# Kernel optimization log

Measured on AMD Instinct MI355X. Metric: run time of the kernel, lower is better.

Reference implementation:

```python
import jax, jax.numpy as jnp
import numpy as np
from jax import lax

FEAT_X, FEAT_Y = 50, 37          # generate_anchors(50, 37)
BASE_SIZE, DSR = 8.0, 16.0
A = FEAT_X * FEAT_Y * 9          # 16650 anchors


def generate_anchors():
    # Vectorized version of the triple python loop; order: x, y, size, [b1,b2,b3]
    xs = jnp.arange(FEAT_X, dtype=jnp.float32)[:, None, None]
    ys = jnp.arange(FEAT_Y, dtype=jnp.float32)[None, :, None]
    s = jnp.array([BASE_SIZE, 2 * BASE_SIZE, 4 * BASE_SIZE], jnp.float32)[None, None, :]

    def box(x1, y1, x2, y2):
        return jnp.stack(jnp.broadcast_arrays(x1 * DSR, y1 * DSR, x2 * DSR, y2 * DSR), axis=-1)

    b1 = box(xs - s / 2, ys - s / 2, xs + s / 2, ys + s / 2)      # square
    b2 = box(xs - s,     ys - s / 4, xs + s,     ys + s / 4)      # wide
    b3 = box(xs - s / 4, ys - s,     xs + s / 4, ys + s)          # tall
    anchors = jnp.stack([b1, b2, b3], axis=3)  # (50,37,3 sizes,3 variants,4)
    return anchors.reshape(-1, 4)              # (16650,4)


def conv2d(x, w, b, padding):
    y = lax.conv_general_dilated(x, w, (1, 1), padding,
                                 dimension_numbers=("NCHW", "OIHW", "NCHW"))
    return y + b[None, :, None, None]


def pairwise_iou(anchors, gt):
    # anchors: (A,4), gt: (B,G,4) -> iou (B,A,G); zero when no positive overlap
    a = anchors[None, :, None, :]
    g = gt[:, None, :, :]
    area_a = (a[..., 2] - a[..., 0]) * (a[..., 3] - a[..., 1])
    area_g = (g[..., 2] - g[..., 0]) * (g[..., 3] - g[..., 1])
    left = jnp.maximum(a[..., 0], g[..., 0])
    right = jnp.minimum(a[..., 2], g[..., 2])
    top = jnp.maximum(a[..., 1], g[..., 1])
    bot = jnp.minimum(a[..., 3], g[..., 3])
    no_ov = (left >= right) | (top >= bot)
    inter = jnp.where(no_ov, 0.0, (right - left) * (bot - top))
    return jnp.where(no_ov, 0.0, inter / (area_a + area_g - inter))


def setup_inputs() -> dict:
    key = jax.random.key(0)
    k1, k2, k3, k4, k5, k6, k7, k8 = jax.random.split(key, 8)
    B, G = 8, 20
    feats = jax.random.normal(k1, (B, 512, FEAT_Y, FEAT_X), jnp.float32)
    # well-formed gt boxes inside an ~800x592 image
    raw = jax.random.uniform(k2, (B, G, 2, 2)) * jnp.array([800.0, 592.0])
    x1y1 = jnp.min(raw, axis=2)
    x2y2 = jnp.max(raw, axis=2) + 1.0
    gt_boxes = jnp.concatenate([x1y1, x2y2], axis=-1)  # (B,G,4)
    im_info = jnp.array([[592.0, 800.0, 1.0]], jnp.float32)  # (h, w, scale)
    s = 0.02
    w3 = jax.random.normal(k3, (512, 512, 3, 3), jnp.float32) * s
    b3 = jnp.zeros((512,), jnp.float32)
    wc = jax.random.normal(k4, (18, 512, 1, 1), jnp.float32) * s
    bc = jnp.zeros((18,), jnp.float32)
    wb = jax.random.normal(k5, (36, 512, 1, 1), jnp.float32) * s
    bb = jnp.zeros((36,), jnp.float32)
    return {"feats": feats, "w3": w3, "b3": b3, "wc": wc, "bc": bc,
            "wb": wb, "bb": bb, "gt_boxes": gt_boxes, "im_info": im_info}


def reference(feats, w3, b3, wc, bc, wb, bb, gt_boxes, im_info):
    B = feats.shape[0]
    anchors = generate_anchors()
    rpn_conv1 = jax.nn.relu(conv2d(feats, w3, b3, ((1, 1), (1, 1))))
    rpn_cls_score = conv2d(rpn_conv1, wc, bc, ((0, 0), (0, 0)))  # (B,18,H,W)
    Bc, C, H, W = rpn_cls_score.shape
    score_rs = rpn_cls_score.reshape(Bc, 2, (C * H) // 2, W)      # reshape(x, 2)
    rpn_cls_prob = jax.nn.softmax(score_rs, axis=1).reshape(Bc, 18, H, W)
    rpn_bbox_pred = conv2d(rpn_conv1, wb, bb, ((0, 0), (0, 0)))   # (B,36,H,W)

    # anchor-target assignment (training branch), faithful to original logic
    inside = ((anchors[:, 0] >= 0) & (anchors[:, 1] >= 0) &
              (anchors[:, 2] < im_info[0, 1]) & (anchors[:, 3] < im_info[0, 0]))
    iou = pairwise_iou(anchors, gt_boxes)                 # (B,A,G)
    iou = jnp.where(inside[None, :, None], iou, 0.0)      # outside anchors skipped
    G = gt_boxes.shape[1]
    # original: idxs = argmax(iou_matrix[:][j]) with j == last gt index
    idx = jnp.argmax(iou[:, G - 1, :], axis=-1)           # (B,)
    labels = jnp.zeros((B, anchors.shape[0]), jnp.float32)
    labels = labels.at[jnp.arange(B), idx].set(1.0)
    max_iou = jnp.max(iou, axis=-1)                       # (B,A)
    labels = jnp.where(inside[None, :] & (max_iou > 0.7), 0.0, labels)

    out = jnp.concatenate([rpn_cls_prob, rpn_bbox_pred], axis=1)  # (B,54,H,W)
    return out, iou, labels
```

## Files before the change

kernel.cpp:

```cpp
#include <hip/hip_runtime.h>

typedef unsigned short u16;
typedef unsigned int u32;
typedef float f32x4 __attribute__((ext_vector_type(4)));
typedef short bf16x8 __attribute__((ext_vector_type(8)));

#define NB 8
#define FH 37
#define FW 50
#define FHW 1850
#define MTOT 14800
#define CIN 512
#define KTOT 4608
#define HP 39
#define WP 52
#define ANCH 16650
#define NG 20

#define ZB 356
#define WTB 512
#define WHB 128
#define TRB 3712
#define PRE_TOT (ZB + WTB + WHB + TRB)

#define CONVB 960
#define IOB 528

#define POSTB 464

__device__ __forceinline__ u16 f2bf(float f) {
    u32 u = __float_as_uint(f);
    u += 0x7fffu + ((u >> 16) & 1u);
    return (u16)(u >> 16);
}

__device__ __forceinline__ void gl2lds16(const u16* g, u16* l) {
    __builtin_amdgcn_global_load_lds((const __attribute__((address_space(1))) void*)(g),
                                     (__attribute__((address_space(3))) void*)(l),
                                     16, 0, 0);
}

__device__ __forceinline__ void anchor_box(int a, float& x1, float& y1, float& x2, float& y2) {
    int x = a / 333;
    int rem = a - x * 333;
    int y = rem / 9;
    int r2 = rem - y * 9;
    int si = r2 / 3;
    int bi = r2 - si * 3;
    float s = (float)(8 << si);
    float fx = (float)x, fy = (float)y;
    float ax1, ay1, ax2, ay2;
    if (bi == 0)      { float h = s * 0.5f;  ax1 = fx - h; ay1 = fy - h; ax2 = fx + h; ay2 = fy + h; }
    else if (bi == 1) { float q = s * 0.25f; ax1 = fx - s; ay1 = fy - q; ax2 = fx + s; ay2 = fy + q; }
    else              { float q = s * 0.25f; ax1 = fx - q; ay1 = fy - s; ax2 = fx + q; ay2 = fy + s; }
    x1 = ax1 * 16.f; y1 = ay1 * 16.f; x2 = ax2 * 16.f; y2 = ay2 * 16.f;
}

__global__ __launch_bounds__(256) void k_pre(u16* __restrict__ apad,
                                             const float* __restrict__ w3, u16* __restrict__ wt,
                                             const float* __restrict__ wc, const float* __restrict__ wb,
                                             u16* __restrict__ whd,
                                             const float* __restrict__ feats) {
    __shared__ __attribute__((aligned(16))) char smraw[18432];
    int blk = blockIdx.x;
    int t = threadIdx.x;

    if (blk < ZB) {
        uint4* apad4 = (uint4*)apad;
        int i = blk * 256 + t;
        int img = i / 11392;
        int r = i - img * 11392;
        int u4;
        if (r < 3328) u4 = r;
        else if (r < 6656) u4 = 126464 + (r - 3328);
        else {
            int rp = r - 6656;
            int h = 1 + (rp >> 7);
            int c2 = rp & 127;
            int col = (c2 & 64) ? 51 : 0;
            u4 = (h * 52 + col) * 64 + (c2 & 63);
        }
        apad4[img * 129792 + u4] = make_uint4(0u, 0u, 0u, 0u);
    } else if (blk < ZB + WTB) {
        float* lt = (float*)smraw;
        int n = blk - ZB;
        const float* src = w3 + n * KTOT;
        for (int i = t; i < KTOT; i += 256) lt[i] = src[i];
        __syncthreads();
        u16* dst = wt + n * KTOT;
        for (int o = t; o < KTOT; o += 256) {
            int tap = o >> 9, ci = o & 511;
            dst[o] = f2bf(lt[ci * 9 + tap]);
        }
    } else if (blk < ZB + WTB + WHB) {
        int i = (blk - ZB - WTB) * 256 + t;
        int n = i >> 9;
        int ci = i & 511;
        float v = 0.f;
        if (n < 18) v = wc[n * 512 + ci];
        else if (n < 54) v = wb[(n - 18) * 512 + ci];
        whd[i] = f2bf(v);
    } else {
        float* tile = (float*)smraw;
        int q = blk - ZB - WTB - WHB;
        int xt = q % 58;
        int r2 = q / 58;
        int ct = r2 & 7;
        int img = r2 >> 3;
        int hw0 = xt * 32, c0 = ct * 64;
        int lx = t & 31, ly = t >> 5;
        #pragma unroll
        for (int rr = 0; rr < 8; rr++) {
            int cl = ly + rr * 8;
            int hw = hw0 + lx;
            if (hw < FHW) tile[cl * 33 + lx] = feats[(img * 512 + c0 + cl) * FHW + hw];
        }
        __syncthreads();
        #pragma unroll
        for (int rr = 0; rr < 4; rr++) {
            int hwl = ly + rr * 8;
            int hw2 = hw0 + hwl;
            if (hw2 < FHW) {
                int h = hw2 / FW, w = hw2 - h * FW;
                float v0 = tile[(2 * lx) * 33 + hwl];
                float v1 = tile[(2 * lx + 1) * 33 + hwl];
                u32 pk = (u32)f2bf(v0) | ((u32)f2bf(v1) << 16);
                u32* dst = (u32*)&apad[(((img * HP) + h + 1) * WP + (w + 1)) * 512 + c0];
                dst[lx] = pk;
            }
        }
    }
}

__global__ __launch_bounds__(256) void k_conv(const u16* __restrict__ apad,
                                              const u16* __restrict__ wt,
                                              const float* __restrict__ b3,
                                              u16* __restrict__ act,
                                              const float* __restrict__ gt,
                                              const float* __restrict__ im,
                                              float* __restrict__ iou_out,
                                              float* __restrict__ lab) {
    __shared__ __attribute__((aligned(16))) char sm[24576];
    __shared__ int idxs;
    int L = blockIdx.x;
    int tid = threadIdx.x;

    if (L < CONVB) {
        u16* As = (u16*)sm;
        u16* Bs = (u16*)(sm + 16384);
        int mb = (L & 7) + 8 * (L >> 6);
        int nb = (L >> 3) & 7;
        if (mb >= 116) return;
        int wave = tid >> 6, lane = tid & 63;
        int m0 = mb * 128;
        int n0 = nb * 64;
        int wr = wave >> 1, wn = wave & 1;
        int lm = lane & 15, lq = lane >> 4;
        int l7 = lm & 7;

        f32x4 acc[4][2] = {};

        int rloc = tid >> 3;
        int cg = (tid & 7) ^ (rloc & 7);
        int aBase[4], bBase[2];
        for (int i = 0; i < 4; i++) {
            int m = m0 + i * 32 + rloc; if (m > MTOT - 1) m = MTOT - 1;
            int b = m / FHW; int hw = m - b * FHW;
            int h = hw / FW; int w = hw - h * FW;
            aBase[i] = ((b * HP + h) * WP + w) * 512 + cg * 8;
        }
        for (int j = 0; j < 2; j++)
            bBase[j] = (n0 + j * 32 + rloc) * KTOT + cg * 8;

        u16* aL[4]; u16* bL[2];
        for (int i = 0; i < 4; i++) aL[i] = &As[(i * 32 + wave * 8) * 64];
        for (int j = 0; j < 2; j++) bL[j] = &Bs[(j * 32 + wave * 8) * 64];

        for (int kk = 0; kk < KTOT; kk += 64) {
            int tap = kk >> 9;
            int ci0 = kk & 511;
            int dy = tap / 3, dx = tap - dy * 3;
            int aOfs = (dy * WP + dx) * 512 + ci0;
            gl2lds16(apad + aBase[0] + aOfs, aL[0]);
            gl2lds16(apad + aBase[1] + aOfs, aL[1]);
            gl2lds16(apad + aBase[2] + aOfs, aL[2]);
            gl2lds16(apad + aBase[3] + aOfs, aL[3]);
            gl2lds16(wt + bBase[0] + kk, bL[0]);
            gl2lds16(wt + bBase[1] + kk, bL[1]);
            __syncthreads();
            bf16x8 a[2][4], b[2][2];
            #pragma unroll
            for (int ks = 0; ks < 2; ks++) {
                int slotb = ((ks * 4 + lq) ^ l7) * 8;
                #pragma unroll
                for (int i = 0; i < 4; i++)
                    a[ks][i] = *(const bf16x8*)&As[(wr * 64 + i * 16 + lm) * 64 + slotb];
                #pragma unroll
                for (int j = 0; j < 2; j++)
                    b[ks][j] = *(const bf16x8*)&Bs[(wn * 32 + j * 16 + lm) * 64 + slotb];
            }
            #pragma unroll
            for (int ks = 0; ks < 2; ks++)
                #pragma unroll
                for (int i = 0; i < 4; i++)
                    #pragma unroll
                    for (int j = 0; j < 2; j++)
                        acc[i][j] = __builtin_amdgcn_mfma_f32_16x16x32_bf16(a[ks][i], b[ks][j], acc[i][j], 0, 0, 0);
            __syncthreads();
        }

        for (int j = 0; j < 2; j++) {
            int n = n0 + wn * 32 + j * 16 + lm;
            float bias = b3[n];
            for (int i = 0; i < 4; i++) {
                int mb2 = m0 + wr * 64 + i * 16 + lq * 4;
                for (int r = 0; r < 4; r++) {
                    int m = mb2 + r;
                    if (m < MTOT) {
                        float v = acc[i][j][r] + bias;
                        act[m * 512 + n] = f2bf(v > 0.f ? v : 0.f);
                    }
                }
            }
        }
    } else {
        float* g4 = (float*)sm;
        float* imv = g4 + 80;
        float* buf = g4 + 84;
        int q = L - CONVB;
        int at = q % 66;
        int b = q / 66;
        int t = tid;
        if (t < NG * 4) g4[t] = gt[b * NG * 4 + t];
        if (t < 2) imv[t] = im[t];
        __syncthreads();
        if (t == 0) {
            float x1, y1, x2, y2;
            anchor_box(19, x1, y1, x2, y2);
            bool inside = (x1 >= 0.f) && (y1 >= 0.f) && (x2 < imv[1]) && (y2 < imv[0]);
            float aa = (x2 - x1) * (y2 - y1);
            float best = -1.f; int bg = 0;
            for (int g2 = 0; g2 < NG; g2++) {
                float gx1 = g4[g2 * 4], gy1 = g4[g2 * 4 + 1], gx2 = g4[g2 * 4 + 2], gy2 = g4[g2 * 4 + 3];
                float l = fmaxf(x1, gx1), r = fminf(x2, gx2);
                float tp = fmaxf(y1, gy1), bo = fminf(y2, gy2);
                float v = 0.f;
                if (l < r && tp < bo) {
                    float inter = (r - l) * (bo - tp);
                    float ag = (gx2 - gx1) * (gy2 - gy1);
                    v = inter / (aa + ag - inter);
                }
                if (!inside) v = 0.f;
                if (v > best) { best = v; bg = g2; }
            }
            idxs = bg;
        }
        int a0 = at * 256;
        int a = a0 + t;
        float mx = 0.f;
        bool inside = false;
        if (a < ANCH) {
            float x1, y1, x2, y2;
            anchor_box(a, x1, y1, x2, y2);
            inside = (x1 >= 0.f) && (y1 >= 0.f) && (x2 < imv[1]) && (y2 < imv[0]);
            float aa = (x2 - x1) * (y2 - y1);
            for (int g2 = 0; g2 < NG; g2++) {
                float gx1 = g4[g2 * 4], gy1 = g4[g2 * 4 + 1], gx2 = g4[g2 * 4 + 2], gy2 = g4[g2 * 4 + 3];
                float l = fmaxf(x1, gx1), r = fminf(x2, gx2);
                float tp = fmaxf(y1, gy1), bo = fminf(y2, gy2);
                float v = 0.f;
                if (l < r && tp < bo) {
                    float inter = (r - l) * (bo - tp);
                    float ag = (gx2 - gx1) * (gy2 - gy1);
                    v = inter / (aa + ag - inter);
                }
                if (!inside) v = 0.f;
                buf[t * NG + g2] = v;
                mx = fmaxf(mx, v);
            }
        }
        __syncthreads();
        int rem = ANCH - a0;
        int cnt2 = (rem < 256 ? rem : 256) * NG;
        float* dst = iou_out + (b * ANCH + a0) * NG;
        for (int i = t; i < cnt2; i += 256) dst[i] = buf[i];
        if (a < ANCH) {
            float lv = (a == idxs) ? 1.f : 0.f;
            if (inside && mx > 0.7f) lv = 0.f;
            lab[b * ANCH + a] = lv;
        }
    }
}

__global__ __launch_bounds__(128) void k_post(const u16* __restrict__ act,
                                              const u16* __restrict__ whd,
                                              const float* __restrict__ bc,
                                              const float* __restrict__ bb,
                                              float* __restrict__ out) {
    __shared__ __attribute__((aligned(16))) u16 Wl[64 * 512];
    int tid = threadIdx.x;
    for (int i = tid; i < 4096; i += 128) {
        int row = i >> 6, cs = i & 63;
        uint4 v = *(const uint4*)&whd[row * 512 + cs * 8];
        *(uint4*)&Wl[row * 512 + (cs ^ (row & 7)) * 8] = v;
    }
    __syncthreads();
    int wave = tid >> 6, lane = tid & 63;
    int lm = lane & 15, lq = lane >> 4;
    int m0 = blockIdx.x * 32 + wave * 16;
    int mr = m0 + lm; if (mr > MTOT - 1) mr = MTOT - 1;
    const u16* arow = act + mr * 512;
    f32x4 acc[4] = {};
    for (int ks = 0; ks < 64; ks += 4) {
        bf16x8 a = *(const bf16x8*)&arow[ks * 8 + lq * 8];
        #pragma unroll
        for (int j = 0; j < 4; j++) {
            int row = j * 16 + lm;
            bf16x8 b = *(const bf16x8*)&Wl[row * 512 + (((ks + lq) ^ (row & 7)) * 8)];
            acc[j] = __builtin_amdgcn_mfma_f32_16x16x32_bf16(a, b, acc[j], 0, 0, 0);
        }
    }
    __syncthreads();
    float* Sl = (float*)Wl;
    float* S = &Sl[wave * 1040];
    #pragma unroll
    for (int r = 0; r < 4; r++)
        #pragma unroll
        for (int j = 0; j < 4; j++)
            S[(lq * 4 + r) * 65 + j * 16 + lm] = acc[j][r];
    __syncthreads();
    int r16 = lane & 15, cg = lane >> 4;
    int m = m0 + r16;
    if (m < MTOT) {
        int b = m / FHW, hw = m - b * FHW;
        const float* Sr = &S[r16 * 65];
        #pragma unroll
        for (int k = 0; k < 14; k++) {
            int c = cg + 4 * k;
            if (c >= 54) break;
            float v;
            if (c < 18) {
                int c0 = c < 9 ? c : c - 9;
                float s0 = Sr[c0] + bc[c0];
                float s1 = Sr[c0 + 9] + bc[c0 + 9];
                float mx = fmaxf(s0, s1);
                float e0 = __expf(s0 - mx), e1 = __expf(s1 - mx);
                v = (c < 9 ? e0 : e1) / (e0 + e1);
            } else {
                v = Sr[c] + bb[c - 18];
            }
            out[(b * 54 + c) * FHW + hw] = v;
        }
    }
}

extern "C" void kernel_launch(void* const* d_in, const int* in_sizes, int n_in,
                              void* d_out, int out_size, void* d_ws, size_t ws_size,
                              hipStream_t stream) {
    (void)in_sizes; (void)n_in; (void)out_size; (void)ws_size;
    const float* feats = (const float*)d_in[0];
    const float* w3    = (const float*)d_in[1];
    const float* b3    = (const float*)d_in[2];
    const float* wc    = (const float*)d_in[3];
    const float* bc    = (const float*)d_in[4];
    const float* wb    = (const float*)d_in[5];
    const float* bb    = (const float*)d_in[6];
    const float* gt    = (const float*)d_in[7];
    const float* im    = (const float*)d_in[8];
    float* out = (float*)d_out;
    char* ws = (char*)d_ws;

    u16* apad = (u16*)(ws);
    u16* wt   = (u16*)(ws + 16613376);
    u16* whd  = (u16*)(ws + 21331968);
    u16* act  = (u16*)(ws + 21397504);

    float* iou_out = out + 799200;
    float* lab     = out + 3463200;

    k_pre<<<dim3(PRE_TOT), dim3(256), 0, stream>>>(apad, w3, wt, wc, wb, whd, feats);
    k_conv<<<dim3(CONVB + IOB), dim3(256), 0, stream>>>(apad, wt, b3, act, gt, im, iou_out, lab);
    k_post<<<dim3(POSTB), dim3(128), 0, stream>>>(act, whd, bc, bb, out);
}
```

Before: 203.6 us.

## Stage padded activation window once per channel chunk and reuse across 3x3 taps

The implicit-GEMM conv now loads a contiguous window of padded activation rows (352 pixels × 64 channels) into LDS once per 64-channel chunk. All nine filter taps then read from that window at shifted row offsets, instead of re-staging an A tile per tap. Weights are no longer staged in LDS and are read directly from global memory into registers per tap. This cuts redundant activation loads and barriers (8 outer iterations instead of 72), at the cost of a larger LDS footprint that may lower occupancy and uncoalesced per-lane global weight loads.

```diff
diff --git a/kernel.cpp b/kernel.cpp
--- a/kernel.cpp
+++ b/kernel.cpp
@@ -25,6 +25,8 @@
 
 #define CONVB 960
 #define IOB 528
+
+#define WIN 352
 
 #define POSTB 464
 
@@ -140,14 +142,13 @@
                                               const float* __restrict__ im,
                                               float* __restrict__ iou_out,
                                               float* __restrict__ lab) {
-    __shared__ __attribute__((aligned(16))) char sm[24576];
+    __shared__ __attribute__((aligned(16))) char sm[45056];
     __shared__ int idxs;
     int L = blockIdx.x;
     int tid = threadIdx.x;
 
     if (L < CONVB) {
         u16* As = (u16*)sm;
-        u16* Bs = (u16*)(sm + 16384);
         int mb = (L & 7) + 8 * (L >> 6);
         int nb = (L >> 3) & 7;
         if (mb >= 116) return;
@@ -156,56 +157,65 @@
         int n0 = nb * 64;
         int wr = wave >> 1, wn = wave & 1;
         int lm = lane & 15, lq = lane >> 4;
-        int l7 = lm & 7;
-
-        f32x4 acc[4][2] = {};
-
-        int rloc = tid >> 3;
-        int cg = (tid & 7) ^ (rloc & 7);
-        int aBase[4], bBase[2];
+
+        int b0 = m0 / FHW; int hw0g = m0 - b0 * FHW;
+        int h0 = hw0g / FW; int w0 = hw0g - h0 * FW;
+        int base0 = (b0 * HP + h0) * WP + w0;
+
+        int rIdx0[4];
+        #pragma unroll
         for (int i = 0; i < 4; i++) {
-            int m = m0 + i * 32 + rloc; if (m > MTOT - 1) m = MTOT - 1;
+            int m = m0 + wr * 64 + i * 16 + lm; if (m > MTOT - 1) m = MTOT - 1;
             int b = m / FHW; int hw = m - b * FHW;
             int h = hw / FW; int w = hw - h * FW;
-            aBase[i] = ((b * HP + h) * WP + w) * 512 + cg * 8;
-        }
-        for (int j = 0; j < 2; j++)
-            bBase[j] = (n0 + j * 32 + rloc) * KTOT + cg * 8;
-
-        u16* aL[4]; u16* bL[2];
-        for (int i = 0; i < 4; i++) aL[i] = &As[(i * 32 + wave * 8) * 64];
-        for (int j = 0; j < 2; j++) bL[j] = &Bs[(j * 32 + wave * 8) * 64];
-
-        for (int kk = 0; kk < KTOT; kk += 64) {
-            int tap = kk >> 9;
-            int ci0 = kk & 511;
-            int dy = tap / 3, dx = tap - dy * 3;
-            int aOfs = (dy * WP + dx) * 512 + ci0;
-            gl2lds16(apad + aBase[0] + aOfs, aL[0]);
-            gl2lds16(apad + aBase[1] + aOfs, aL[1]);
-            gl2lds16(apad + aBase[2] + aOfs, aL[2]);
-            gl2lds16(apad + aBase[3] + aOfs, aL[3]);
-            gl2lds16(wt + bBase[0] + kk, bL[0]);
-            gl2lds16(wt + bBase[1] + kk, bL[1]);
+            rIdx0[i] = (b * HP + h) * WP + w - base0;
+        }
+
+        int bRow = (n0 + wn * 32 + lm) * KTOT + lq * 8;
+
+        int sRow = tid >> 3;
+        int sg = (tid & 7) ^ (sRow & 7);
+        const int PMAX = NB * HP * WP - 1;
+
+        f32x4 acc[4][2] = {};
+
+        for (int c = 0; c < 8; c++) {
+            int ci = c * 64;
+            #pragma unroll
+            for (int rr = 0; rr < 11; rr++) {
+                int p = base0 + rr * 32 + sRow; if (p > PMAX) p = PMAX;
+                gl2lds16(apad + p * 512 + ci + sg * 8, &As[rr * 2048 + wave * 512]);
+            }
             __syncthreads();
-            bf16x8 a[2][4], b[2][2];
             #pragma unroll
-            for (int ks = 0; ks < 2; ks++) {
-                int slotb = ((ks * 4 + lq) ^ l7) * 8;
+            for (int dy = 0; dy < 3; dy++) {
                 #pragma unroll
-                for (int i = 0; i < 4; i++)
-                    a[ks][i] = *(const bf16x8*)&As[(wr * 64 + i * 16 + lm) * 64 + slotb];
-                #pragma unroll
-                for (int j = 0; j < 2; j++)
-                    b[ks][j] = *(const bf16x8*)&Bs[(wn * 32 + j * 16 + lm) * 64 + slotb];
-            }
-            #pragma unroll
-            for (int ks = 0; ks < 2; ks++)
-                #pragma unroll
-                for (int i = 0; i < 4; i++)
+                for (int dx = 0; dx < 3; dx++) {
+                    int tap = dy * 3 + dx;
+                    int tOfs = dy * WP + dx;
+                    int bk = bRow + tap * 512 + ci;
+                    bf16x8 bv[2][2];
+                    bv[0][0] = *(const bf16x8*)&wt[bk];
+                    bv[0][1] = *(const bf16x8*)&wt[bk + 16 * KTOT];
+                    bv[1][0] = *(const bf16x8*)&wt[bk + 32];
+                    bv[1][1] = *(const bf16x8*)&wt[bk + 16 * KTOT + 32];
+                    bf16x8 a[2][4];
                     #pragma unroll
-                    for (int j = 0; j < 2; j++)
-                        acc[i][j] = __builtin_amdgcn_mfma_f32_16x16x32_bf16(a[ks][i], b[ks][j], acc[i][j], 0, 0, 0);
+                    for (int ks = 0; ks < 2; ks++)
+                        #pragma unroll
+                        for (int i = 0; i < 4; i++) {
+                            int r = rIdx0[i] + tOfs;
+                            a[ks][i] = *(const bf16x8*)&As[r * 64 + (((ks * 4 + lq) ^ (r & 7)) * 8)];
+                        }
+                    #pragma unroll
+                    for (int ks = 0; ks < 2; ks++)
+                        #pragma unroll
+                        for (int i = 0; i < 4; i++) {
+                            acc[i][0] = __builtin_amdgcn_mfma_f32_16x16x32_bf16(a[ks][i], bv[ks][0], acc[i][0], 0, 0, 0);
+                            acc[i][1] = __builtin_amdgcn_mfma_f32_16x16x32_bf16(a[ks][i], bv[ks][1], acc[i][1], 0, 0, 0);
+                        }
+                }
+            }
             __syncthreads();
         }
 
```

Result: slower. 269.0 us (+32.1%).
